# Performance work log

Measured on AMD Instinct MI355X. Metric: run time of the kernel, lower is better.

The kernel has to match this reference:

```python
import jax, jax.numpy as jnp
import numpy as np

B, H_HIST, S_DIM, HID, G, K, A = 1024, 16384, 32, 64, 10, 4, 8


def setup_inputs() -> dict:
    key = jax.random.key(0)
    ks = jax.random.split(key, 12)
    inp = {
        'state_batch': jax.random.normal(ks[0], (B, S_DIM), jnp.float32),
        'state_history_batch': jax.random.normal(ks[1], (H_HIST, S_DIM), jnp.float32),
        'joint_action_history_batch': jax.random.normal(ks[2], (H_HIST, G, A), jnp.float32),
        # per-abstract-agent encoder MLP: Linear(S->H) + ReLU, Linear(H->H) + ReLU, Linear(H->H) + ReLU
        'W0': jax.random.normal(ks[3], (K, S_DIM, HID), jnp.float32) / np.sqrt(S_DIM),
        'b0': jax.random.normal(ks[4], (K, HID), jnp.float32) * 0.01,
        'W1': jax.random.normal(ks[5], (K, HID, HID), jnp.float32) / np.sqrt(HID),
        'b1': jax.random.normal(ks[6], (K, HID), jnp.float32) * 0.01,
        'W2': jax.random.normal(ks[7], (K, HID, HID), jnp.float32) / np.sqrt(HID),
        'b2': jax.random.normal(ks[8], (K, HID), jnp.float32) * 0.01,
        'assignment_matrix': jnp.ones((G, K), jnp.float32),
    }
    return inp


def _encode(x, W0, b0, W1, b1, W2, b2):
    # x: [N, S_DIM] shared across K encoders -> [K, N, HID]
    h = jax.nn.relu(jnp.einsum('ni,kio->kno', x, W0) + b0[:, None, :])
    h = jax.nn.relu(jnp.einsum('kni,kio->kno', h, W1) + b1[:, None, :])
    h = jax.nn.relu(jnp.einsum('kni,kio->kno', h, W2) + b2[:, None, :])
    return h


def reference(state_batch, state_history_batch, joint_action_history_batch,
              W0, b0, W1, b1, W2, b2, assignment_matrix):
    enc_s = _encode(state_batch, W0, b0, W1, b1, W2, b2)            # [K, B, HID]
    enc_h = _encode(state_history_batch, W0, b0, W1, b1, W2, b2)    # [K, H, HID]
    # per (abstract agent k, batch item b): softmax over history of <enc_h, enc_s>
    attn = jax.nn.softmax(jnp.einsum('khd,kbd->kbh', enc_h, enc_s), axis=-1)  # [K, B, H]
    # weighted action aggregation: [H,G,A] contracted over H
    abs_pred = jnp.einsum('kbh,hga->kbga', attn, joint_action_history_batch)  # [K, B, G, A]
    soft_assign = jax.nn.softmax(assignment_matrix, axis=-1)                  # [G, K]
    out = jnp.einsum('gk,kbga->bga', soft_assign, abs_pred)                   # [B, G, A]
    return out
```

## Files before the change

kernel.cpp:

```cpp
#include <hip/hip_runtime.h>
#include <stdint.h>

#define B_SZ 1024
#define H_SZ 16384
#define SD   32
#define HID  64
#define G_SZ 10
#define K_SZ 4
#define A_SZ 8
#define VA   80

typedef float f32x4  __attribute__((ext_vector_type(4)));
typedef short bf16x8 __attribute__((ext_vector_type(8)));

__device__ inline short f2bf(float a) {
    unsigned u = __float_as_uint(a);
    return (short)((u + 0x7FFFu + ((u >> 16) & 1u)) >> 16);
}
__device__ inline float bf2f(short s) {
    return __uint_as_float(((unsigned)(unsigned short)s) << 16);
}
__device__ inline void split_bf(float v, short& hi, short& lo) {
    hi = f2bf(v);
    lo = f2bf(v - bf2f(hi));
}
__device__ inline int pk_bf16(float a, float b) {
    unsigned ua = __float_as_uint(a), ub = __float_as_uint(b);
    ua = (ua + 0x7FFFu + ((ua >> 16) & 1u)) >> 16;
    ub = (ub + 0x7FFFu + ((ub >> 16) & 1u)) >> 16;
    return (int)(ua | (ub << 16));
}

__global__ __launch_bounds__(256, 2) void k_encode(
    const float* __restrict__ state, const float* __restrict__ hist,
    const float* __restrict__ act,
    const float* __restrict__ W0, const float* __restrict__ b0,
    const float* __restrict__ W1, const float* __restrict__ b1,
    const float* __restrict__ W2, const float* __restrict__ b2,
    short* __restrict__ enc_s_h, short* __restrict__ enc_s_l,
    short* __restrict__ enc_h_h, short* __restrict__ enc_h_l,
    short* __restrict__ vt_h, short* __restrict__ vt_l)
{
    __shared__ __align__(16) short smem[28672];
    const int bid = blockIdx.x;
    const int t = threadIdx.x;

    if (bid >= 1088) {
        short* tile_h = smem;
        short* tile_l = smem + 10752;
        const int h0 = (bid - 1088) * 128;
        for (int i = 0; i < 40; ++i) {
            int idx = t + i * 256;
            float v = act[(size_t)h0 * VA + idx];
            int h = idx / VA, c = idx - h * VA;
            short hh, ll; split_bf(v, hh, ll);
            tile_h[h * 84 + c] = hh;
            tile_l[h * 84 + c] = ll;
        }
        __syncthreads();
        for (int i = 0; i < 5; ++i) {
            int j = t + i * 256;
            int va = j >> 4, hc = j & 15;
            union { short s[8]; uint4 v; } uh, ul;
            #pragma unroll
            for (int uu = 0; uu < 8; ++uu) {
                uh.s[uu] = tile_h[(hc * 8 + uu) * 84 + va];
                ul.s[uu] = tile_l[(hc * 8 + uu) * 84 + va];
            }
            *(uint4*)(vt_h + (size_t)va * H_SZ + h0 + hc * 8) = uh.v;
            *(uint4*)(vt_l + (size_t)va * H_SZ + h0 + hc * 8) = ul.v;
        }
        return;
    }

    const int k = bid / 272;
    const int tl = bid % 272;
    const float* X;
    short *dst_h, *dst_l;
    if (tl < 16) {
        X = state + (size_t)tl * 64 * SD;
        dst_h = enc_s_h + ((size_t)k * B_SZ + tl * 64) * HID;
        dst_l = enc_s_l + ((size_t)k * B_SZ + tl * 64) * HID;
    } else {
        X = hist + (size_t)(tl - 16) * 64 * SD;
        dst_h = enc_h_h + ((size_t)k * H_SZ + (tl - 16) * 64) * HID;
        dst_l = enc_h_l + ((size_t)k * H_SZ + (tl - 16) * 64) * HID;
    }

    short* xt_h  = smem;
    short* xt_l  = smem + 2560;
    short* wt0_h = smem + 5120;
    short* wt0_l = smem + 7680;
    short* hb2_h = smem;
    short* hb2_l = smem + 4608;
    short* wt1_h = smem + 10240;
    short* wt1_l = smem + 14848;
    short* hb1_h = smem + 19456;
    short* hb1_l = smem + 24064;
    short* wt2_h = smem + 19456;
    short* wt2_l = smem + 24064;

    const float* W0k = W0 + k * (SD * HID);
    const float* W1k = W1 + k * (HID * HID);
    const float* W2k = W2 + k * (HID * HID);

    {
        int r = t >> 2, c0 = (t & 3) * 8;
        const float* src = X + r * SD + c0;
        #pragma unroll
        for (int u = 0; u < 8; ++u) {
            short hh, ll; split_bf(src[u], hh, ll);
            xt_h[r * 40 + c0 + u] = hh;
            xt_l[r * 40 + c0 + u] = ll;
        }
    }
    {
        int i = t >> 3, j0 = (t & 7) * 8;
        #pragma unroll
        for (int u = 0; u < 8; ++u) {
            short hh, ll; split_bf(W0k[i * HID + j0 + u], hh, ll);
            wt0_h[(j0 + u) * 40 + i] = hh;
            wt0_l[(j0 + u) * 40 + i] = ll;
        }
    }
    {
        int i = t >> 2, j0 = (t & 3) * 16;
        #pragma unroll
        for (int u = 0; u < 16; ++u) {
            short hh, ll; split_bf(W1k[i * HID + j0 + u], hh, ll);
            wt1_h[(j0 + u) * 72 + i] = hh;
            wt1_l[(j0 + u) * 72 + i] = ll;
        }
    }
    __syncthreads();

    const int w = t >> 6, l15 = t & 15, quad = (t >> 4) & 3;
    const f32x4 fz = {0.f, 0.f, 0.f, 0.f};

    {
        bf16x8 xa_h = *(const bf16x8*)(xt_h + (w * 16 + l15) * 40 + quad * 8);
        bf16x8 xa_l = *(const bf16x8*)(xt_l + (w * 16 + l15) * 40 + quad * 8);
        const float* b0k = b0 + k * HID;
        #pragma unroll
        for (int tt = 0; tt < 4; ++tt) {
            bf16x8 wf_h = *(const bf16x8*)(wt0_h + (l15 + 16 * tt) * 40 + quad * 8);
            bf16x8 wf_l = *(const bf16x8*)(wt0_l + (l15 + 16 * tt) * 40 + quad * 8);
            f32x4 c = __builtin_amdgcn_mfma_f32_16x16x32_bf16(xa_h, wf_h, fz, 0, 0, 0);
            c = __builtin_amdgcn_mfma_f32_16x16x32_bf16(xa_l, wf_h, c, 0, 0, 0);
            c = __builtin_amdgcn_mfma_f32_16x16x32_bf16(xa_h, wf_l, c, 0, 0, 0);
            float bias = b0k[l15 + 16 * tt];
            #pragma unroll
            for (int r = 0; r < 4; ++r) {
                float f = fmaxf(c[r] + bias, 0.f);
                short hh, ll; split_bf(f, hh, ll);
                hb1_h[(w * 16 + quad * 4 + r) * 72 + l15 + 16 * tt] = hh;
                hb1_l[(w * 16 + quad * 4 + r) * 72 + l15 + 16 * tt] = ll;
            }
        }
    }
    __syncthreads();
    {
        bf16x8 ha0_h = *(const bf16x8*)(hb1_h + (w * 16 + l15) * 72 + quad * 8);
        bf16x8 ha0_l = *(const bf16x8*)(hb1_l + (w * 16 + l15) * 72 + quad * 8);
        bf16x8 ha1_h = *(const bf16x8*)(hb1_h + (w * 16 + l15) * 72 + 32 + quad * 8);
        bf16x8 ha1_l = *(const bf16x8*)(hb1_l + (w * 16 + l15) * 72 + 32 + quad * 8);
        const float* b1k = b1 + k * HID;
        #pragma unroll
        for (int tt = 0; tt < 4; ++tt) {
            bf16x8 wfa_h = *(const bf16x8*)(wt1_h + (l15 + 16 * tt) * 72 + quad * 8);
            bf16x8 wfa_l = *(const bf16x8*)(wt1_l + (l15 + 16 * tt) * 72 + quad * 8);
            bf16x8 wfb_h = *(const bf16x8*)(wt1_h + (l15 + 16 * tt) * 72 + 32 + quad * 8);
            bf16x8 wfb_l = *(const bf16x8*)(wt1_l + (l15 + 16 * tt) * 72 + 32 + quad * 8);
            f32x4 c = __builtin_amdgcn_mfma_f32_16x16x32_bf16(ha0_h, wfa_h, fz, 0, 0, 0);
            c = __builtin_amdgcn_mfma_f32_16x16x32_bf16(ha1_h, wfb_h, c, 0, 0, 0);
            c = __builtin_amdgcn_mfma_f32_16x16x32_bf16(ha0_l, wfa_h, c, 0, 0, 0);
            c = __builtin_amdgcn_mfma_f32_16x16x32_bf16(ha1_l, wfb_h, c, 0, 0, 0);
            c = __builtin_amdgcn_mfma_f32_16x16x32_bf16(ha0_h, wfa_l, c, 0, 0, 0);
            c = __builtin_amdgcn_mfma_f32_16x16x32_bf16(ha1_h, wfb_l, c, 0, 0, 0);
            float bias = b1k[l15 + 16 * tt];
            #pragma unroll
            for (int r = 0; r < 4; ++r) {
                float f = fmaxf(c[r] + bias, 0.f);
                short hh, ll; split_bf(f, hh, ll);
                hb2_h[(w * 16 + quad * 4 + r) * 72 + l15 + 16 * tt] = hh;
                hb2_l[(w * 16 + quad * 4 + r) * 72 + l15 + 16 * tt] = ll;
            }
        }
    }
    __syncthreads();
    {
        int i = t >> 2, j0 = (t & 3) * 16;
        #pragma unroll
        for (int u = 0; u < 16; ++u) {
            short hh, ll; split_bf(W2k[i * HID + j0 + u], hh, ll);
            wt2_h[(j0 + u) * 72 + i] = hh;
            wt2_l[(j0 + u) * 72 + i] = ll;
        }
    }
    __syncthreads();
    {
        bf16x8 ha0_h = *(const bf16x8*)(hb2_h + (w * 16 + l15) * 72 + quad * 8);
        bf16x8 ha0_l = *(const bf16x8*)(hb2_l + (w * 16 + l15) * 72 + quad * 8);
        bf16x8 ha1_h = *(const bf16x8*)(hb2_h + (w * 16 + l15) * 72 + 32 + quad * 8);
        bf16x8 ha1_l = *(const bf16x8*)(hb2_l + (w * 16 + l15) * 72 + 32 + quad * 8);
        const float* b2k = b2 + k * HID;
        #pragma unroll
        for (int tt = 0; tt < 4; ++tt) {
            bf16x8 wfa_h = *(const bf16x8*)(wt2_h + (l15 + 16 * tt) * 72 + quad * 8);
            bf16x8 wfa_l = *(const bf16x8*)(wt2_l + (l15 + 16 * tt) * 72 + quad * 8);
            bf16x8 wfb_h = *(const bf16x8*)(wt2_h + (l15 + 16 * tt) * 72 + 32 + quad * 8);
            bf16x8 wfb_l = *(const bf16x8*)(wt2_l + (l15 + 16 * tt) * 72 + 32 + quad * 8);
            f32x4 c = __builtin_amdgcn_mfma_f32_16x16x32_bf16(ha0_h, wfa_h, fz, 0, 0, 0);
            c = __builtin_amdgcn_mfma_f32_16x16x32_bf16(ha1_h, wfb_h, c, 0, 0, 0);
            c = __builtin_amdgcn_mfma_f32_16x16x32_bf16(ha0_l, wfa_h, c, 0, 0, 0);
            c = __builtin_amdgcn_mfma_f32_16x16x32_bf16(ha1_l, wfb_h, c, 0, 0, 0);
            c = __builtin_amdgcn_mfma_f32_16x16x32_bf16(ha0_h, wfa_l, c, 0, 0, 0);
            c = __builtin_amdgcn_mfma_f32_16x16x32_bf16(ha1_h, wfb_l, c, 0, 0, 0);
            float bias = b2k[l15 + 16 * tt];
            #pragma unroll
            for (int r = 0; r < 4; ++r) {
                float f = fmaxf(c[r] + bias, 0.f);
                short hh, ll; split_bf(f, hh, ll);
                dst_h[(w * 16 + quad * 4 + r) * HID + l15 + 16 * tt] = hh;
                dst_l[(w * 16 + quad * 4 + r) * HID + l15 + 16 * tt] = ll;
            }
        }
    }
}

template<int NCt>
__global__ __launch_bounds__(256, 2) void k_flash(
    const short* __restrict__ enc_s_h, const short* __restrict__ enc_s_l,
    const short* __restrict__ enc_h_h, const short* __restrict__ enc_h_l,
    const short* __restrict__ vth, const short* __restrict__ vtl,
    float* __restrict__ Pm, float* __restrict__ Pl, float* __restrict__ Pacc)
{
    constexpr int CHt = H_SZ / NCt;
    __shared__ __align__(16) short kh_h[32 * 72];
    __shared__ __align__(16) short kh_l[32 * 72];
    __shared__ __align__(16) short vts_h[80 * 40];
    __shared__ __align__(16) short vts_l[80 * 40];

    const int bid = blockIdx.x;
    const int r8 = bid & 7, j = bid >> 3;
    const int mtile = j & 7, grp = j >> 3;
    const int idx = grp * 8 + r8;
    const int k = idx / NCt, chunk = idx % NCt;
    const int t = threadIdx.x, w = t >> 6, l15 = t & 15, quad = (t >> 4) & 3;
    const short* ehk_h = enc_h_h + (size_t)k * H_SZ * HID;
    const short* ehk_l = enc_h_l + (size_t)k * H_SZ * HID;
    const int h_base = chunk * CHt;
    const int q0 = mtile * 128 + w * 32;
    const float L2E = 1.44269504f;
    const f32x4 fz = {0.f, 0.f, 0.f, 0.f};

    bf16x8 qh[2][2], ql[2][2];
    #pragma unroll
    for (int sub = 0; sub < 2; ++sub)
        #pragma unroll
        for (int kb = 0; kb < 2; ++kb) {
            size_t off = ((size_t)k * B_SZ + q0 + sub * 16 + l15) * HID + kb * 32 + quad * 8;
            qh[sub][kb] = *(const bf16x8*)(enc_s_h + off);
            ql[sub][kb] = *(const bf16x8*)(enc_s_l + off);
        }

    f32x4 acc[2][5];
    #pragma unroll
    for (int s = 0; s < 2; ++s)
        #pragma unroll
        for (int tt = 0; tt < 5; ++tt) acc[s][tt] = fz;
    float mrun[2] = {-__builtin_inff(), -__builtin_inff()};
    float lrun[2] = {0.f, 0.f};

    const int krr = t >> 3, kcc = (t & 7) * 8;
    const int vrw = t >> 2, vcl = (t & 3) * 8;
    const int vrw2 = 64 + (t >> 2);

    uint4 pkh, pkl, pvh, pvl, pv2h, pv2l;
    auto load_tile = [&](int h0) {
        pkh = *(const uint4*)(ehk_h + (size_t)(h0 + krr) * HID + kcc);
        pkl = *(const uint4*)(ehk_l + (size_t)(h0 + krr) * HID + kcc);
        pvh = *(const uint4*)(vth + (size_t)vrw * H_SZ + h0 + vcl);
        pvl = *(const uint4*)(vtl + (size_t)vrw * H_SZ + h0 + vcl);
        if (t < 64) {
            pv2h = *(const uint4*)(vth + (size_t)vrw2 * H_SZ + h0 + vcl);
            pv2l = *(const uint4*)(vtl + (size_t)vrw2 * H_SZ + h0 + vcl);
        }
    };
    auto store_tile = [&]() {
        *(uint4*)(kh_h + krr * 72 + kcc) = pkh;
        *(uint4*)(kh_l + krr * 72 + kcc) = pkl;
        *(uint4*)(vts_h + vrw * 40 + vcl) = pvh;
        *(uint4*)(vts_l + vrw * 40 + vcl) = pvl;
        if (t < 64) {
            *(uint4*)(vts_h + vrw2 * 40 + vcl) = pv2h;
            *(uint4*)(vts_l + vrw2 * 40 + vcl) = pv2l;
        }
    };

    load_tile(h_base);
    store_tile();

    for (int it = 0; it < CHt / 32; ++it) {
        const int h0 = h_base + it * 32;
        __syncthreads();
        if (it + 1 < CHt / 32) load_tile(h0 + 32);

        bf16x8 ka_h[2][2], ka_l[2][2];
        #pragma unroll
        for (int hs = 0; hs < 2; ++hs)
            #pragma unroll
            for (int kb = 0; kb < 2; ++kb) {
                ka_h[hs][kb] = *(const bf16x8*)(kh_h + (hs * 16 + l15) * 72 + kb * 32 + quad * 8);
                ka_l[hs][kb] = *(const bf16x8*)(kh_l + (hs * 16 + l15) * 72 + kb * 32 + quad * 8);
            }

        bf16x8 pfv[2];
        #pragma unroll
        for (int sub = 0; sub < 2; ++sub) {
            __builtin_amdgcn_s_setprio(1);
            f32x4 slo = __builtin_amdgcn_mfma_f32_16x16x32_bf16(ka_h[0][0], qh[sub][0], fz, 0, 0, 0);
            slo = __builtin_amdgcn_mfma_f32_16x16x32_bf16(ka_h[0][1], qh[sub][1], slo, 0, 0, 0);
            slo = __builtin_amdgcn_mfma_f32_16x16x32_bf16(ka_l[0][0], qh[sub][0], slo, 0, 0, 0);
            slo = __builtin_amdgcn_mfma_f32_16x16x32_bf16(ka_l[0][1], qh[sub][1], slo, 0, 0, 0);
            slo = __builtin_amdgcn_mfma_f32_16x16x32_bf16(ka_h[0][0], ql[sub][0], slo, 0, 0, 0);
            slo = __builtin_amdgcn_mfma_f32_16x16x32_bf16(ka_h[0][1], ql[sub][1], slo, 0, 0, 0);
            f32x4 shi = __builtin_amdgcn_mfma_f32_16x16x32_bf16(ka_h[1][0], qh[sub][0], fz, 0, 0, 0);
            shi = __builtin_amdgcn_mfma_f32_16x16x32_bf16(ka_h[1][1], qh[sub][1], shi, 0, 0, 0);
            shi = __builtin_amdgcn_mfma_f32_16x16x32_bf16(ka_l[1][0], qh[sub][0], shi, 0, 0, 0);
            shi = __builtin_amdgcn_mfma_f32_16x16x32_bf16(ka_l[1][1], qh[sub][1], shi, 0, 0, 0);
            shi = __builtin_amdgcn_mfma_f32_16x16x32_bf16(ka_h[1][0], ql[sub][0], shi, 0, 0, 0);
            shi = __builtin_amdgcn_mfma_f32_16x16x32_bf16(ka_h[1][1], ql[sub][1], shi, 0, 0, 0);
            __builtin_amdgcn_s_setprio(0);

            float tm = fmaxf(fmaxf(fmaxf(slo[0], slo[1]), fmaxf(slo[2], slo[3])),
                             fmaxf(fmaxf(shi[0], shi[1]), fmaxf(shi[2], shi[3])));
            tm = fmaxf(tm, __shfl_xor(tm, 16));
            tm = fmaxf(tm, __shfl_xor(tm, 32));
            if (__any(tm > mrun[sub])) {
                float mnew = fmaxf(mrun[sub], tm);
                float alpha = exp2f((mrun[sub] - mnew) * L2E);
                lrun[sub] *= alpha;
                #pragma unroll
                for (int tt = 0; tt < 5; ++tt) acc[sub][tt] = acc[sub][tt] * alpha;
                mrun[sub] = mnew;
            }
            float m = mrun[sub];
            float p0 = exp2f((slo[0] - m) * L2E), p1 = exp2f((slo[1] - m) * L2E);
            float p2 = exp2f((slo[2] - m) * L2E), p3 = exp2f((slo[3] - m) * L2E);
            float p4 = exp2f((shi[0] - m) * L2E), p5 = exp2f((shi[1] - m) * L2E);
            float p6 = exp2f((shi[2] - m) * L2E), p7 = exp2f((shi[3] - m) * L2E);
            float ps = (p0 + p1) + (p2 + p3) + (p4 + p5) + (p6 + p7);
            ps += __shfl_xor(ps, 16);
            ps += __shfl_xor(ps, 32);
            lrun[sub] += ps;

            int plo01 = pk_bf16(p0, p1), plo23 = pk_bf16(p2, p3);
            int phi01 = pk_bf16(p4, p5), phi23 = pk_bf16(p6, p7);
            union { int i[4]; bf16x8 v; } pf;
            #pragma unroll
            for (int jj = 0; jj < 4; ++jj) {
                int src = (((2 * quad + (jj >> 1)) & 3) << 4) + l15;
                int glo = __shfl((jj & 1) ? plo23 : plo01, src);
                int ghi = __shfl((jj & 1) ? phi23 : phi01, src);
                pf.i[jj] = (quad >= 2) ? ghi : glo;
            }
            pfv[sub] = pf.v;
        }

        __builtin_amdgcn_s_setprio(1);
        #pragma unroll
        for (int tt = 0; tt < 5; ++tt) {
            bf16x8 vh = *(const bf16x8*)(vts_h + (l15 + 16 * tt) * 40 + quad * 8);
            bf16x8 vl = *(const bf16x8*)(vts_l + (l15 + 16 * tt) * 40 + quad * 8);
            acc[0][tt] = __builtin_amdgcn_mfma_f32_16x16x32_bf16(vh, pfv[0], acc[0][tt], 0, 0, 0);
            acc[0][tt] = __builtin_amdgcn_mfma_f32_16x16x32_bf16(vl, pfv[0], acc[0][tt], 0, 0, 0);
            acc[1][tt] = __builtin_amdgcn_mfma_f32_16x16x32_bf16(vh, pfv[1], acc[1][tt], 0, 0, 0);
            acc[1][tt] = __builtin_amdgcn_mfma_f32_16x16x32_bf16(vl, pfv[1], acc[1][tt], 0, 0, 0);
        }
        __builtin_amdgcn_s_setprio(0);

        __syncthreads();
        if (it + 1 < CHt / 32) store_tile();
    }

    const int qg = k * B_SZ + q0;
    #pragma unroll
    for (int sub = 0; sub < 2; ++sub) {
        int q = qg + sub * 16 + l15;
        if (quad == 0) {
            Pm[chunk * 4096 + q] = mrun[sub];
            Pl[chunk * 4096 + q] = lrun[sub];
        }
        #pragma unroll
        for (int tt = 0; tt < 5; ++tt)
            #pragma unroll
            for (int r = 0; r < 4; ++r) {
                int va = tt * 16 + quad * 4 + r;
                Pacc[((size_t)chunk * VA + va) * 4096 + q] = acc[sub][tt][r];
            }
    }
}

template<int NCt>
__global__ __launch_bounds__(256) void k_reduce1(
    const float* __restrict__ Pm, const float* __restrict__ Pl,
    const float* __restrict__ Pacc, float* __restrict__ O)
{
    const int bid = blockIdx.x;
    const int qb = bid / 10, vc = bid - qb * 10;
    const int t = threadIdx.x;
    const int q = qb * 64 + (t & 63);
    const int va0 = vc * 8 + (t >> 6) * 2;
    const float L2E = 1.44269504f;

    float mc[NCt];
    float M = -__builtin_inff();
    #pragma unroll
    for (int c = 0; c < NCt; ++c) { mc[c] = Pm[c * 4096 + q]; M = fmaxf(M, mc[c]); }
    float L = 0.f;
    float o0 = 0.f, o1 = 0.f;
    #pragma unroll
    for (int c = 0; c < NCt; ++c) {
        float wv = exp2f((mc[c] - M) * L2E);
        L += wv * Pl[c * 4096 + q];
        o0 += wv * Pacc[((size_t)c * VA + va0) * 4096 + q];
        o1 += wv * Pacc[((size_t)c * VA + va0 + 1) * 4096 + q];
    }
    float inv = 1.f / L;
    O[(size_t)q * VA + va0]     = o0 * inv;
    O[(size_t)q * VA + va0 + 1] = o1 * inv;
}

__global__ __launch_bounds__(256) void k_reduce2(
    const float* __restrict__ O, const float* __restrict__ assign,
    float* __restrict__ out)
{
    const int idx = blockIdx.x * 256 + threadIdx.x;
    const int b = idx / VA, va = idx - b * VA, g = va >> 3;
    const float L2E = 1.44269504f;
    float a0 = assign[g * K_SZ + 0], a1 = assign[g * K_SZ + 1];
    float a2 = assign[g * K_SZ + 2], a3 = assign[g * K_SZ + 3];
    float mx = fmaxf(fmaxf(a0, a1), fmaxf(a2, a3));
    float e0 = exp2f((a0 - mx) * L2E), e1 = exp2f((a1 - mx) * L2E);
    float e2 = exp2f((a2 - mx) * L2E), e3 = exp2f((a3 - mx) * L2E);
    float inv = 1.f / (e0 + e1 + e2 + e3);
    float o = e0 * O[((size_t)(0 * B_SZ + b)) * VA + va]
            + e1 * O[((size_t)(1 * B_SZ + b)) * VA + va]
            + e2 * O[((size_t)(2 * B_SZ + b)) * VA + va]
            + e3 * O[((size_t)(3 * B_SZ + b)) * VA + va];
    out[idx] = o * inv;
}

extern "C" void kernel_launch(void* const* d_in, const int* in_sizes, int n_in,
                              void* d_out, int out_size, void* d_ws, size_t ws_size,
                              hipStream_t stream)
{
    const float* state  = (const float*)d_in[0];
    const float* hist   = (const float*)d_in[1];
    const float* act    = (const float*)d_in[2];
    const float* W0     = (const float*)d_in[3];
    const float* b0     = (const float*)d_in[4];
    const float* W1     = (const float*)d_in[5];
    const float* b1     = (const float*)d_in[6];
    const float* W2     = (const float*)d_in[7];
    const float* b2     = (const float*)d_in[8];
    const float* assign = (const float*)d_in[9];
    float* out = (float*)d_out;

    char* ws = (char*)d_ws;
    short* enc_s_h = (short*)(ws);
    short* enc_s_l = (short*)(ws + 524288);
    short* enc_h_h = (short*)(ws + 1048576);
    short* enc_h_l = (short*)(ws + 9437184);
    short* vt_h    = (short*)(ws + 17825792);
    short* vt_l    = (short*)(ws + 20447232);
    const size_t base = 23068672;

    const size_t need32 = base + 32ull * (32768 + 1310720) + 1310720;
    const int nc = (ws_size >= need32) ? 32 : 16;

    float* Pm   = (float*)(ws + base);
    float* Pl   = (float*)(ws + base + (size_t)nc * 16384);
    float* Pacc = (float*)(ws + base + (size_t)nc * 32768);
    float* O    = (float*)(ws + base + (size_t)nc * 32768 + (size_t)nc * 1310720);

    k_encode<<<1216, 256, 0, stream>>>(state, hist, act, W0, b0, W1, b1, W2, b2,
                                       enc_s_h, enc_s_l, enc_h_h, enc_h_l, vt_h, vt_l);
    if (nc == 32) {
        k_flash<32><<<1024, 256, 0, stream>>>(enc_s_h, enc_s_l, enc_h_h, enc_h_l,
                                              vt_h, vt_l, Pm, Pl, Pacc);
        k_reduce1<32><<<640, 256, 0, stream>>>(Pm, Pl, Pacc, O);
    } else {
        k_flash<16><<<512, 256, 0, stream>>>(enc_s_h, enc_s_l, enc_h_h, enc_h_l,
                                             vt_h, vt_l, Pm, Pl, Pacc);
        k_reduce1<16><<<640, 256, 0, stream>>>(Pm, Pl, Pacc, O);
    }
    k_reduce2<<<320, 256, 0, stream>>>(O, assign, out);
}
```

Before: 182.3 us.

## Double-buffer flash tiles via direct global-to-LDS loads with swizzled layouts

The flash kernel now stages K and V tiles with global_load_lds (direct DMA into LDS) into double-buffered shared arrays, replacing the register-staged load/store with padded strides. To avoid LDS bank conflicts without padding, the encoder writes enc_h and the transposed action matrix in XOR-swizzled column order, and the flash reads use matching swizzled offsets. Launch bounds are raised to allow 4 blocks per CU, and the QK MFMAs for both row-halves are grouped ahead of the softmax. This adds coupling between the encoder's output layout and the flash kernel's reads, plus register pressure from the higher occupancy target.

```diff
diff --git a/kernel.cpp b/kernel.cpp
--- a/kernel.cpp
+++ b/kernel.cpp
@@ -29,6 +29,11 @@
     ua = (ua + 0x7FFFu + ((ua >> 16) & 1u)) >> 16;
     ub = (ub + 0x7FFFu + ((ub >> 16) & 1u)) >> 16;
     return (int)(ua | (ub << 16));
+}
+__device__ inline void dma16(const short* g, const short* l) {
+    __builtin_amdgcn_global_load_lds(
+        (const __attribute__((address_space(1))) unsigned int*)g,
+        (__attribute__((address_space(3))) unsigned int*)l, 16, 0, 0);
 }
 
 __global__ __launch_bounds__(256, 2) void k_encode(
@@ -67,14 +72,17 @@
                 uh.s[uu] = tile_h[(hc * 8 + uu) * 84 + va];
                 ul.s[uu] = tile_l[(hc * 8 + uu) * 84 + va];
             }
-            *(uint4*)(vt_h + (size_t)va * H_SZ + h0 + hc * 8) = uh.v;
-            *(uint4*)(vt_l + (size_t)va * H_SZ + h0 + hc * 8) = ul.v;
+            int t32 = hc >> 2, g = hc & 3;
+            int gp = g ^ ((va >> 1) & 3);
+            *(uint4*)(vt_h + (size_t)va * H_SZ + h0 + t32 * 32 + gp * 8) = uh.v;
+            *(uint4*)(vt_l + (size_t)va * H_SZ + h0 + t32 * 32 + gp * 8) = ul.v;
         }
         return;
     }
 
     const int k = bid / 272;
     const int tl = bid % 272;
+    const bool swz = (tl >= 16);
     const float* X;
     short *dst_h, *dst_l;
     if (tl < 16) {
@@ -221,32 +229,37 @@
             for (int r = 0; r < 4; ++r) {
                 float f = fmaxf(c[r] + bias, 0.f);
                 short hh, ll; split_bf(f, hh, ll);
-                dst_h[(w * 16 + quad * 4 + r) * HID + l15 + 16 * tt] = hh;
-                dst_l[(w * 16 + quad * 4 + r) * HID + l15 + 16 * tt] = ll;
+                int row = w * 16 + quad * 4 + r;
+                int c0 = l15 + 16 * tt;
+                int col = swz ? ((((c0 >> 3) ^ (row & 7)) << 3) | (c0 & 7)) : c0;
+                dst_h[row * HID + col] = hh;
+                dst_l[row * HID + col] = ll;
             }
         }
     }
 }
 
 template<int NCt>
-__global__ __launch_bounds__(256, 2) void k_flash(
+__global__ __launch_bounds__(256, 4) void k_flash(
     const short* __restrict__ enc_s_h, const short* __restrict__ enc_s_l,
     const short* __restrict__ enc_h_h, const short* __restrict__ enc_h_l,
     const short* __restrict__ vth, const short* __restrict__ vtl,
     float* __restrict__ Pm, float* __restrict__ Pl, float* __restrict__ Pacc)
 {
     constexpr int CHt = H_SZ / NCt;
-    __shared__ __align__(16) short kh_h[32 * 72];
-    __shared__ __align__(16) short kh_l[32 * 72];
-    __shared__ __align__(16) short vts_h[80 * 40];
-    __shared__ __align__(16) short vts_l[80 * 40];
+    constexpr int NT = CHt / 32;
+    __shared__ __align__(16) short kbh[2][32 * 64];
+    __shared__ __align__(16) short kbl[2][32 * 64];
+    __shared__ __align__(16) short vbh[2][80 * 32];
+    __shared__ __align__(16) short vbl[2][80 * 32];
 
     const int bid = blockIdx.x;
     const int r8 = bid & 7, j = bid >> 3;
     const int mtile = j & 7, grp = j >> 3;
     const int idx = grp * 8 + r8;
     const int k = idx / NCt, chunk = idx % NCt;
-    const int t = threadIdx.x, w = t >> 6, l15 = t & 15, quad = (t >> 4) & 3;
+    const int t = threadIdx.x, w = t >> 6, lane = t & 63;
+    const int l15 = t & 15, quad = (t >> 4) & 3;
     const short* ehk_h = enc_h_h + (size_t)k * H_SZ * HID;
     const short* ehk_l = enc_h_l + (size_t)k * H_SZ * HID;
     const int h_base = chunk * CHt;
@@ -272,67 +285,64 @@
     float mrun[2] = {-__builtin_inff(), -__builtin_inff()};
     float lrun[2] = {0.f, 0.f};
 
-    const int krr = t >> 3, kcc = (t & 7) * 8;
-    const int vrw = t >> 2, vcl = (t & 3) * 8;
-    const int vrw2 = 64 + (t >> 2);
-
-    uint4 pkh, pkl, pvh, pvl, pv2h, pv2l;
-    auto load_tile = [&](int h0) {
-        pkh = *(const uint4*)(ehk_h + (size_t)(h0 + krr) * HID + kcc);
-        pkl = *(const uint4*)(ehk_l + (size_t)(h0 + krr) * HID + kcc);
-        pvh = *(const uint4*)(vth + (size_t)vrw * H_SZ + h0 + vcl);
-        pvl = *(const uint4*)(vtl + (size_t)vrw * H_SZ + h0 + vcl);
-        if (t < 64) {
-            pv2h = *(const uint4*)(vth + (size_t)vrw2 * H_SZ + h0 + vcl);
-            pv2l = *(const uint4*)(vtl + (size_t)vrw2 * H_SZ + h0 + vcl);
-        }
+    const int koff0 = l15 * 64 + (((quad)     ^ (l15 & 7)) << 3);
+    const int koff1 = l15 * 64 + (((4 + quad) ^ (l15 & 7)) << 3);
+    const int vof   = l15 * 32 + ((quad ^ ((l15 >> 1) & 3)) << 3);
+
+    auto vseg = [&](int seg, int h0, int nb) {
+        bool hi = seg < 5;
+        int sb = hi ? seg : seg - 5;
+        int va = sb * 16 + (lane >> 2);
+        const short* src = (hi ? vth : vtl) + (size_t)va * H_SZ + h0 + (lane & 3) * 8;
+        const short* dst = (hi ? &vbh[nb][0] : &vbl[nb][0]) + sb * 512;
+        dma16(src, dst);
     };
-    auto store_tile = [&]() {
-        *(uint4*)(kh_h + krr * 72 + kcc) = pkh;
-        *(uint4*)(kh_l + krr * 72 + kcc) = pkl;
-        *(uint4*)(vts_h + vrw * 40 + vcl) = pvh;
-        *(uint4*)(vts_l + vrw * 40 + vcl) = pvl;
-        if (t < 64) {
-            *(uint4*)(vts_h + vrw2 * 40 + vcl) = pv2h;
-            *(uint4*)(vts_l + vrw2 * 40 + vcl) = pv2l;
-        }
+    auto stage = [&](int h0, int nb) {
+        dma16(ehk_h + (size_t)h0 * 64 + w * 512 + lane * 8, &kbh[nb][w * 512]);
+        dma16(ehk_l + (size_t)h0 * 64 + w * 512 + lane * 8, &kbl[nb][w * 512]);
+        vseg(w, h0, nb);
+        vseg(w + 4, h0, nb);
+        if (w < 2) vseg(w + 8, h0, nb);
     };
 
-    load_tile(h_base);
-    store_tile();
-
-    for (int it = 0; it < CHt / 32; ++it) {
-        const int h0 = h_base + it * 32;
-        __syncthreads();
-        if (it + 1 < CHt / 32) load_tile(h0 + 32);
-
-        bf16x8 ka_h[2][2], ka_l[2][2];
-        #pragma unroll
-        for (int hs = 0; hs < 2; ++hs)
-            #pragma unroll
-            for (int kb = 0; kb < 2; ++kb) {
-                ka_h[hs][kb] = *(const bf16x8*)(kh_h + (hs * 16 + l15) * 72 + kb * 32 + quad * 8);
-                ka_l[hs][kb] = *(const bf16x8*)(kh_l + (hs * 16 + l15) * 72 + kb * 32 + quad * 8);
-            }
+    stage(h_base, 0);
+    asm volatile("s_waitcnt vmcnt(0)" ::: "memory");
+    __syncthreads();
+
+    for (int it = 0; it < NT; ++it) {
+        const int cur = it & 1;
+        if (it + 1 < NT) stage(h_base + (it + 1) * 32, cur ^ 1);
+
+        const short* kch = kbh[cur];
+        const short* kcl = kbl[cur];
+        const short* vch = vbh[cur];
+        const short* vcl = vbl[cur];
+
+        f32x4 S[2][2];
+        __builtin_amdgcn_s_setprio(1);
+        #pragma unroll
+        for (int hs = 0; hs < 2; ++hs) {
+            bf16x8 kah0 = *(const bf16x8*)(kch + hs * 1024 + koff0);
+            bf16x8 kah1 = *(const bf16x8*)(kch + hs * 1024 + koff1);
+            bf16x8 kal0 = *(const bf16x8*)(kcl + hs * 1024 + koff0);
+            bf16x8 kal1 = *(const bf16x8*)(kcl + hs * 1024 + koff1);
+            #pragma unroll
+            for (int sub = 0; sub < 2; ++sub) {
+                f32x4 c = __builtin_amdgcn_mfma_f32_16x16x32_bf16(kah0, qh[sub][0], fz, 0, 0, 0);
+                c = __builtin_amdgcn_mfma_f32_16x16x32_bf16(kah1, qh[sub][1], c, 0, 0, 0);
+                c = __builtin_amdgcn_mfma_f32_16x16x32_bf16(kal0, qh[sub][0], c, 0, 0, 0);
+                c = __builtin_amdgcn_mfma_f32_16x16x32_bf16(kal1, qh[sub][1], c, 0, 0, 0);
+                c = __builtin_amdgcn_mfma_f32_16x16x32_bf16(kah0, ql[sub][0], c, 0, 0, 0);
+                c = __builtin_amdgcn_mfma_f32_16x16x32_bf16(kah1, ql[sub][1], c, 0, 0, 0);
+                S[sub][hs] = c;
+            }
+        }
+        __builtin_amdgcn_s_setprio(0);
 
         bf16x8 pfv[2];
         #pragma unroll
         for (int sub = 0; sub < 2; ++sub) {
-            __builtin_amdgcn_s_setprio(1);
-            f32x4 slo = __builtin_amdgcn_mfma_f32_16x16x32_bf16(ka_h[0][0], qh[sub][0], fz, 0, 0, 0);
-            slo = __builtin_amdgcn_mfma_f32_16x16x32_bf16(ka_h[0][1], qh[sub][1], slo, 0, 0, 0);
-            slo = __builtin_amdgcn_mfma_f32_16x16x32_bf16(ka_l[0][0], qh[sub][0], slo, 0, 0, 0);
-            slo = __builtin_amdgcn_mfma_f32_16x16x32_bf16(ka_l[0][1], qh[sub][1], slo, 0, 0, 0);
-            slo = __builtin_amdgcn_mfma_f32_16x16x32_bf16(ka_h[0][0], ql[sub][0], slo, 0, 0, 0);
-            slo = __builtin_amdgcn_mfma_f32_16x16x32_bf16(ka_h[0][1], ql[sub][1], slo, 0, 0, 0);
-            f32x4 shi = __builtin_amdgcn_mfma_f32_16x16x32_bf16(ka_h[1][0], qh[sub][0], fz, 0, 0, 0);
-            shi = __builtin_amdgcn_mfma_f32_16x16x32_bf16(ka_h[1][1], qh[sub][1], shi, 0, 0, 0);
-            shi = __builtin_amdgcn_mfma_f32_16x16x32_bf16(ka_l[1][0], qh[sub][0], shi, 0, 0, 0);
-            shi = __builtin_amdgcn_mfma_f32_16x16x32_bf16(ka_l[1][1], qh[sub][1], shi, 0, 0, 0);
-            shi = __builtin_amdgcn_mfma_f32_16x16x32_bf16(ka_h[1][0], ql[sub][0], shi, 0, 0, 0);
-            shi = __builtin_amdgcn_mfma_f32_16x16x32_bf16(ka_h[1][1], ql[sub][1], shi, 0, 0, 0);
-            __builtin_amdgcn_s_setprio(0);
-
+            f32x4 slo = S[sub][0], shi = S[sub][1];
             float tm = fmaxf(fmaxf(fmaxf(slo[0], slo[1]), fmaxf(slo[2], slo[3])),
                              fmaxf(fmaxf(shi[0], shi[1]), fmaxf(shi[2], shi[3])));
             tm = fmaxf(tm, __shfl_xor(tm, 16));
@@ -371,8 +381,8 @@
         __builtin_amdgcn_s_setprio(1);
         #pragma unroll
         for (int tt = 0; tt < 5; ++tt) {
-            bf16x8 vh = *(const bf16x8*)(vts_h + (l15 + 16 * tt) * 40 + quad * 8);
-            bf16x8 vl = *(const bf16x8*)(vts_l + (l15 + 16 * tt) * 40 + quad * 8);
+            bf16x8 vh = *(const bf16x8*)(vch + vof + tt * 512);
+            bf16x8 vl = *(const bf16x8*)(vcl + vof + tt * 512);
             acc[0][tt] = __builtin_amdgcn_mfma_f32_16x16x32_bf16(vh, pfv[0], acc[0][tt], 0, 0, 0);
             acc[0][tt] = __builtin_amdgcn_mfma_f32_16x16x32_bf16(vl, pfv[0], acc[0][tt], 0, 0, 0);
             acc[1][tt] = __builtin_amdgcn_mfma_f32_16x16x32_bf16(vh, pfv[1], acc[1][tt], 0, 0, 0);
@@ -380,8 +390,8 @@
         }
         __builtin_amdgcn_s_setprio(0);
 
+        asm volatile("s_waitcnt vmcnt(0)" ::: "memory");
         __syncthreads();
-        if (it + 1 < CHt / 32) store_tile();
     }
 
     const int qg = k * B_SZ + q0;
```

Measured after the change: 183.4 us. About the same (+0.6%).
